# Kernel optimization log

Hardware: AMD Instinct MI355X
Metric: run time of the kernel (lower is better)

The kernel has to match this reference:

```python
import jax, jax.numpy as jnp
import numpy as np

N_EMBD = 2048
N_HEAD = 32
HEAD_SIZE = 64          # n_embd // n_head
MIX_DIM = 64            # RWKV-6 time-mix LoRA dim
DECAY_DIM = 128         # RWKV-6 decay LoRA dim
BATCH = 1024
STATE_ROWS = (2 + HEAD_SIZE) * 1  # single block, i = 0


def setup_inputs() -> dict:
    key = jax.random.key(0)
    ks = jax.random.split(key, 32)
    rn = lambda k, shp, s=0.02: jax.random.normal(k, shp, jnp.float32) * s
    d = {}
    d['x'] = jax.random.normal(ks[0], (BATCH, N_EMBD), jnp.float32)
    d['state'] = jax.random.normal(ks[1], (BATCH, STATE_ROWS, N_EMBD), jnp.float32) * 0.1
    d['ln1_w'] = jnp.ones((N_EMBD,), jnp.float32)
    d['ln1_b'] = jnp.zeros((N_EMBD,), jnp.float32)
    d['ln2_w'] = jnp.ones((N_EMBD,), jnp.float32)
    d['ln2_b'] = jnp.zeros((N_EMBD,), jnp.float32)
    d['maa_x'] = rn(ks[2], (N_EMBD,), 0.1)
    d['maa_w'] = rn(ks[3], (N_EMBD,), 0.1)
    d['maa_k'] = rn(ks[4], (N_EMBD,), 0.1)
    d['maa_v'] = rn(ks[5], (N_EMBD,), 0.1)
    d['maa_r'] = rn(ks[6], (N_EMBD,), 0.1)
    d['maa_g'] = rn(ks[7], (N_EMBD,), 0.1)
    d['maa_w1'] = rn(ks[8], (N_EMBD, 5 * MIX_DIM))
    d['maa_w2'] = rn(ks[9], (5, MIX_DIM, N_EMBD))
    d['decay'] = rn(ks[10], (N_EMBD,), 0.5) - 4.0  # typical negative log-decay
    d['decay_w1'] = rn(ks[11], (N_EMBD, DECAY_DIM))
    d['decay_w2'] = rn(ks[12], (DECAY_DIM, N_EMBD))
    d['faaaa'] = rn(ks[13], (N_HEAD, HEAD_SIZE, 1), 0.1)
    d['Wr'] = rn(ks[14], (N_EMBD, N_EMBD))
    d['Wk'] = rn(ks[15], (N_EMBD, N_EMBD))
    d['Wv'] = rn(ks[16], (N_EMBD, N_EMBD))
    d['Wo'] = rn(ks[17], (N_EMBD, N_EMBD))
    d['Wg'] = rn(ks[18], (N_EMBD, N_EMBD))
    d['gn_w'] = jnp.ones((N_EMBD,), jnp.float32)
    d['gn_b'] = jnp.zeros((N_EMBD,), jnp.float32)
    d['ffn_maa_k'] = rn(ks[19], (N_EMBD,), 0.1)
    d['ffn_maa_r'] = rn(ks[20], (N_EMBD,), 0.1)
    d['ffn_Wk'] = rn(ks[21], (N_EMBD, N_EMBD))
    d['ffn_Wr'] = rn(ks[22], (N_EMBD, N_EMBD))
    d['ffn_Wv'] = rn(ks[23], (N_EMBD, N_EMBD))
    d['i'] = 0
    return d


def _ln(x, w, b):
    mu = jnp.mean(x, -1, keepdims=True)
    var = jnp.var(x, -1, keepdims=True)
    return (x - mu) * jax.lax.rsqrt(var + 1e-5) * w + b


def reference(x, state, ln1_w, ln1_b, ln2_w, ln2_b,
              maa_x, maa_w, maa_k, maa_v, maa_r, maa_g, maa_w1, maa_w2,
              decay, decay_w1, decay_w2, faaaa,
              Wr, Wk, Wv, Wo, Wg, gn_w, gn_b,
              ffn_maa_k, ffn_maa_r, ffn_Wk, ffn_Wr, ffn_Wv, i):
    B = x.shape[0]
    H, S = N_HEAD, HEAD_SIZE
    # ---------------- time mixing ----------------
    xn = _ln(x, ln1_w, ln1_b)
    i1 = (2 + S) * i + 1
    sx = state[:, i1] - xn                                  # token shift delta
    xxx = xn + sx * maa_x
    xxx = jnp.tanh(xxx @ maa_w1).reshape(B, 5, 1, MIX_DIM)
    xxx = jnp.matmul(xxx, maa_w2).reshape(B, 5, N_EMBD)     # [B,5,E]
    mw, mk, mv, mr, mg = (xxx[:, j] for j in range(5))
    xw = xn + sx * (maa_w + mw)
    xk = xn + sx * (maa_k + mk)
    xv = xn + sx * (maa_v + mv)
    xr = xn + sx * (maa_r + mr)
    xg = xn + sx * (maa_g + mg)
    w = decay + jnp.tanh(xw @ decay_w1) @ decay_w2          # [B,E]
    w = jnp.exp(-jnp.exp(w.reshape(B, H, S, 1)))            # decay gate
    r = (xr @ Wr.T).reshape(B, H, 1, S)
    k = (xk @ Wk.T).reshape(B, H, S, 1)
    v = (xv @ Wv.T).reshape(B, H, 1, S)
    g = jax.nn.silu(xg @ Wg.T)
    s = state[:, (2 + S) * i + 2:(2 + S) * (i + 1), :].reshape(B, H, S, S)
    a = jnp.matmul(k, v)                                    # [B,H,S,S] outer product
    y = jnp.matmul(r, faaaa * a + s).reshape(B, N_EMBD)     # wkv readout
    # group norm (n_head groups over n_embd channels)
    yg = y.reshape(B, H, S)
    mu = jnp.mean(yg, -1, keepdims=True)
    var = jnp.var(yg, -1, keepdims=True)
    yg = ((yg - mu) * jax.lax.rsqrt(var + 1e-5)).reshape(B, N_EMBD) * gn_w + gn_b
    x1 = x + (yg * g) @ Wo.T
    # ---------------- channel mixing ----------------
    xn2 = _ln(x1, ln2_w, ln2_b)
    i0 = (2 + S) * i
    sx2 = state[:, i0] - xn2
    xk2 = xn2 + sx2 * ffn_maa_k
    xr2 = xn2 + sx2 * ffn_maa_r
    rr = jax.nn.sigmoid(xr2 @ ffn_Wr.T)
    kk = jnp.square(jax.nn.relu(xk2 @ ffn_Wk.T))
    return x1 + rr * (kk @ ffn_Wv.T)
```

## Files before the change

kernel.cpp:

```cpp
#include <hip/hip_runtime.h>
#include <cstdint>
#include <cstddef>

typedef unsigned short u16;
typedef __attribute__((ext_vector_type(8))) short bf16x8;
typedef __attribute__((ext_vector_type(4))) float f32x4;

#define DEV __device__ __forceinline__

DEV u16 f2bf(float f) {
  uint32_t b = __float_as_uint(f);
  b += 0x7fffu + ((b >> 16) & 1u);
  return (u16)(b >> 16);
}
DEV float bf2f(u16 u) { return __uint_as_float(((uint32_t)u) << 16); }

DEV void gl16(const u16* g, u16* l) {
  __builtin_amdgcn_global_load_lds(
      (const __attribute__((address_space(1))) void*)g,
      (__attribute__((address_space(3))) void*)l, 16, 0, 0);
}

struct CvtArgs { const float* s[8]; };

__global__ __launch_bounds__(256) void k_cvt8(CvtArgs a, u16* __restrict__ dst) {
  size_t idx = ((size_t)blockIdx.x * 256 + threadIdx.x) * 8;
  int w = (int)(idx >> 22);
  size_t off = idx & ((1u << 22) - 1);
  const float* s = a.s[w];
  float4 v0 = *(const float4*)(s + off);
  float4 v1 = *(const float4*)(s + off + 4);
  uint4 p; u16* pl = (u16*)&p;
  pl[0] = f2bf(v0.x); pl[1] = f2bf(v0.y); pl[2] = f2bf(v0.z); pl[3] = f2bf(v0.w);
  pl[4] = f2bf(v1.x); pl[5] = f2bf(v1.y); pl[6] = f2bf(v1.z); pl[7] = f2bf(v1.w);
  *(uint4*)(dst + ((size_t)w << 22) + off) = p;
}

__global__ __launch_bounds__(256) void k_cvtT(const float* __restrict__ w1,
                                              const float* __restrict__ w2,
                                              u16* __restrict__ w1t, u16* __restrict__ w2t) {
  int idx = blockIdx.x * 256 + threadIdx.x;
  if (idx < 655360) {
    int n = idx >> 11, k = idx & 2047;
    w1t[idx] = f2bf(w1[(size_t)k * 320 + n]);
  } else {
    int r = idx - 655360;
    int j = r >> 17, q = r & 131071;
    int n = q >> 6, k2 = q & 63;
    w2t[r] = f2bf(w2[((size_t)(j + 1) * 64 + k2) * 2048 + n]);
  }
}

__global__ __launch_bounds__(256) void k_tanhpack(const float* __restrict__ xf,
                                                  u16* __restrict__ xb) {
  int idx = blockIdx.x * 256 + threadIdx.x;
  xb[idx] = f2bf(tanhf(xf[idx]));
}

__global__ __launch_bounds__(256) void k_act(const float* __restrict__ rrf,
                                             const float* __restrict__ kkf,
                                             u16* __restrict__ rr, u16* __restrict__ kk) {
  int gid = blockIdx.x * 256 + threadIdx.x;
  int e0 = (gid & 262143) * 8;
  uint4 p; u16* pl = (u16*)&p;
  if (gid < 262144) {
    float4 v0 = *(const float4*)(rrf + e0);
    float4 v1 = *(const float4*)(rrf + e0 + 4);
    float vv[8] = {v0.x, v0.y, v0.z, v0.w, v1.x, v1.y, v1.z, v1.w};
#pragma unroll
    for (int j = 0; j < 8; ++j) pl[j] = f2bf(1.f / (1.f + __expf(-vv[j])));
    *(uint4*)(rr + e0) = p;
  } else {
    float4 v0 = *(const float4*)(kkf + e0);
    float4 v1 = *(const float4*)(kkf + e0 + 4);
    float vv[8] = {v0.x, v0.y, v0.z, v0.w, v1.x, v1.y, v1.z, v1.w};
#pragma unroll
    for (int j = 0; j < 8; ++j) { float r = vv[j] > 0.f ? vv[j] : 0.f; pl[j] = f2bf(r * r); }
    *(uint4*)(kk + e0) = p;
  }
}

__global__ __launch_bounds__(256) void k_ln_mix1(
    const float* __restrict__ x, const float* __restrict__ state,
    const int* __restrict__ ip,
    const float* __restrict__ lw, const float* __restrict__ lb,
    const float* __restrict__ mx,
    u16* __restrict__ xn_o, u16* __restrict__ sx_o, u16* __restrict__ a1_o,
    float* __restrict__ xxxf) {
  int b = blockIdx.x, t = threadIdx.x;
  float* zf = xxxf + (size_t)b * 320;
  zf[t] = 0.f;
  if (t < 64) zf[256 + t] = 0.f;
  const float* xr = x + (size_t)b * 2048;
  float4 v0 = *(const float4*)(xr + t * 8);
  float4 v1 = *(const float4*)(xr + t * 8 + 4);
  float xv[8] = {v0.x, v0.y, v0.z, v0.w, v1.x, v1.y, v1.z, v1.w};
  float s1 = 0.f, s2 = 0.f;
#pragma unroll
  for (int j = 0; j < 8; ++j) { s1 += xv[j]; s2 += xv[j] * xv[j]; }
#pragma unroll
  for (int off = 32; off; off >>= 1) { s1 += __shfl_xor(s1, off); s2 += __shfl_xor(s2, off); }
  __shared__ float ls1[4], ls2[4];
  int w = t >> 6;
  if ((t & 63) == 0) { ls1[w] = s1; ls2[w] = s2; }
  __syncthreads();
  s1 = ls1[0] + ls1[1] + ls1[2] + ls1[3];
  s2 = ls2[0] + ls2[1] + ls2[2] + ls2[3];
  float mu = s1 * (1.0f / 2048.0f);
  float var = s2 * (1.0f / 2048.0f) - mu * mu;
  float rs = rsqrtf(var + 1e-5f);
  const float* st = state + ((size_t)b * 66 + (size_t)66 * ip[0] + 1) * 2048;
  int e0 = t * 8;
  uint4 xnp, sxp, a1p;
  u16* xnl = (u16*)&xnp; u16* sxl = (u16*)&sxp; u16* a1l = (u16*)&a1p;
#pragma unroll
  for (int j = 0; j < 8; ++j) {
    int e = e0 + j;
    float xn = (xv[j] - mu) * rs * lw[e] + lb[e];
    float sxv = st[e] - xn;
    xnl[j] = f2bf(xn); sxl[j] = f2bf(sxv); a1l[j] = f2bf(xn + sxv * mx[e]);
  }
  size_t o = (size_t)b * 2048 + e0;
  *(uint4*)(xn_o + o) = xnp;
  *(uint4*)(sx_o + o) = sxp;
  *(uint4*)(a1_o + o) = a1p;
}

__global__ __launch_bounds__(256) void k_ln_mix2(
    const float* __restrict__ x1, const float* __restrict__ state,
    const int* __restrict__ ip,
    const float* __restrict__ lw, const float* __restrict__ lb,
    const float* __restrict__ mk, const float* __restrict__ mr,
    u16* __restrict__ xk_o, u16* __restrict__ xr_o, float* __restrict__ out) {
  int b = blockIdx.x, t = threadIdx.x;
  const float* xr = x1 + (size_t)b * 2048;
  float4 v0 = *(const float4*)(xr + t * 8);
  float4 v1 = *(const float4*)(xr + t * 8 + 4);
  float* op = out + (size_t)b * 2048 + t * 8;
  *(float4*)op = v0;
  *(float4*)(op + 4) = v1;
  float xv[8] = {v0.x, v0.y, v0.z, v0.w, v1.x, v1.y, v1.z, v1.w};
  float s1 = 0.f, s2 = 0.f;
#pragma unroll
  for (int j = 0; j < 8; ++j) { s1 += xv[j]; s2 += xv[j] * xv[j]; }
#pragma unroll
  for (int off = 32; off; off >>= 1) { s1 += __shfl_xor(s1, off); s2 += __shfl_xor(s2, off); }
  __shared__ float ls1[4], ls2[4];
  int w = t >> 6;
  if ((t & 63) == 0) { ls1[w] = s1; ls2[w] = s2; }
  __syncthreads();
  s1 = ls1[0] + ls1[1] + ls1[2] + ls1[3];
  s2 = ls2[0] + ls2[1] + ls2[2] + ls2[3];
  float mu = s1 * (1.0f / 2048.0f);
  float var = s2 * (1.0f / 2048.0f) - mu * mu;
  float rs = rsqrtf(var + 1e-5f);
  const float* st = state + ((size_t)b * 66 + (size_t)66 * ip[0] + 0) * 2048;
  int e0 = t * 8;
  uint4 xkp, xrp;
  u16* xkl = (u16*)&xkp; u16* xrl = (u16*)&xrp;
#pragma unroll
  for (int j = 0; j < 8; ++j) {
    int e = e0 + j;
    float xn = (xv[j] - mu) * rs * lw[e] + lb[e];
    float sxv = st[e] - xn;
    xkl[j] = f2bf(xn + sxv * mk[e]);
    xrl[j] = f2bf(xn + sxv * mr[e]);
  }
  size_t o = (size_t)b * 2048 + e0;
  *(uint4*)(xk_o + o) = xkp;
  *(uint4*)(xr_o + o) = xrp;
}

enum { EP_STORE = 0, EP_SILU, EP_MIX, EP_AT, EP_ATSC };

struct GemmDesc {
  const u16* A; const u16* B; void* C;
  const void* p1; const void* p2; const float* pvec;
  int lda, ldb, ldc, N, K, k0, ep;
};
struct GemmBatch { GemmDesc g[4]; int bpg; };

__global__ __launch_bounds__(256, 3) void k_gemm(GemmBatch bat) {
  int gi = blockIdx.x / bat.bpg;
  int bid = blockIdx.x % bat.bpg;
  GemmDesc g = bat.g[gi];
  int ntn = (g.N + 127) >> 7;
  int m0 = (bid / ntn) << 7;
  int n0 = (bid % ntn) << 7;
  __shared__ u16 As[2][128 * 32];
  __shared__ u16 Bs[2][128 * 32];
  int t = threadIdx.x, w = t >> 6, lane = t & 63;
  int wm = w >> 1, wn = w & 1;
  int lr = lane & 15, kb = (lane >> 4) * 8;
  const u16* Ab = g.A + (size_t)(m0 + w * 32 + (lane >> 2)) * g.lda + (lane & 3) * 8;
  const u16* Bb = g.B + (size_t)(n0 + w * 32 + (lane >> 2)) * g.ldb + (lane & 3) * 8;
  int a16 = 16 * g.lda, b16 = 16 * g.ldb;
  int aoff = (w * 32) * 32;
  f32x4 acc[4][4] = {};
  int nt = g.K >> 5;

  auto stage = [&](int buf, int kk) {
    u16* Ad = (u16*)As + buf * 4096 + aoff;
    u16* Bd = (u16*)Bs + buf * 4096 + aoff;
    gl16(Ab + kk, Ad);
    gl16(Ab + kk + a16, Ad + 512);
    gl16(Bb + kk, Bd);
    gl16(Bb + kk + b16, Bd + 512);
  };

  stage(0, g.k0);
  __syncthreads();
  int cur = 0;
  for (int ti = 0; ti < nt; ++ti) {
    if (ti + 1 < nt) stage(cur ^ 1, g.k0 + (ti + 1) * 32);
    const u16* Ac = (const u16*)As + cur * 4096;
    const u16* Bc = (const u16*)Bs + cur * 4096;
    bf16x8 af[4], bfr[4];
#pragma unroll
    for (int m = 0; m < 4; ++m)
      af[m] = *(const bf16x8*)(Ac + (wm * 64 + m * 16 + lr) * 32 + kb);
#pragma unroll
    for (int n = 0; n < 4; ++n)
      bfr[n] = *(const bf16x8*)(Bc + (wn * 64 + n * 16 + lr) * 32 + kb);
#pragma unroll
    for (int m = 0; m < 4; ++m)
#pragma unroll
      for (int n = 0; n < 4; ++n)
        acc[m][n] = __builtin_amdgcn_mfma_f32_16x16x32_bf16(af[m], bfr[n], acc[m][n], 0, 0, 0);
    __syncthreads();
    cur ^= 1;
  }

  int ep = g.ep;
#pragma unroll
  for (int m = 0; m < 4; ++m) {
    int grow0 = m0 + wm * 64 + m * 16 + (lane >> 4) * 4;
#pragma unroll
    for (int n = 0; n < 4; ++n) {
      int gc = n0 + wn * 64 + n * 16 + lr;
      if (gc >= g.N) continue;
#pragma unroll
      for (int q = 0; q < 4; ++q) {
        size_t ci = (size_t)(grow0 + q) * g.ldc + gc;
        float v = acc[m][n][q];
        switch (ep) {
          case EP_STORE: ((u16*)g.C)[ci] = f2bf(v); break;
          case EP_SILU:  ((u16*)g.C)[ci] = f2bf(v / (1.f + __expf(-v))); break;
          case EP_MIX: {
            float xn = bf2f(((const u16*)g.p1)[ci]);
            float sxv = bf2f(((const u16*)g.p2)[ci]);
            ((u16*)g.C)[ci] = f2bf(xn + sxv * (g.pvec[gc] + v));
          } break;
          case EP_AT:   atomicAdd((float*)g.C + ci, v); break;
          case EP_ATSC: atomicAdd((float*)g.C + ci, bf2f(((const u16*)g.p2)[ci]) * v); break;
        }
      }
    }
  }
}

__global__ __launch_bounds__(512, 2) void k_gemm2(GemmBatch bat) {
  extern __shared__ u16 lds[];
  int nwg = gridDim.x;
  int wg0 = blockIdx.x;
  int wg = (wg0 & 7) * (nwg >> 3) + (wg0 >> 3);
  int gi = wg / bat.bpg;
  int bid = wg % bat.bpg;
  GemmDesc g = bat.g[gi];
  int ntn = (g.N + 255) >> 8;
  int m0 = (bid / ntn) << 7;
  int n0 = (bid % ntn) << 8;
  int t = threadIdx.x, wv = t >> 6, lane = t & 63;
  int wm = wv >> 2, wn = wv & 3;
  int lr = lane & 15, hi = lane >> 4;

  const u16* asrc[2]; const u16* bsrc[4];
#pragma unroll
  for (int j = 0; j < 2; ++j) {
    int cid = t + 512 * j, r = cid >> 3, c = cid & 7;
    asrc[j] = g.A + (size_t)(m0 + r) * g.lda + ((c ^ (r & 7)) << 3);
  }
#pragma unroll
  for (int j = 0; j < 4; ++j) {
    int cid = t + 512 * j, r = cid >> 3, c = cid & 7;
    int rowB = n0 + r; if (rowB > g.N - 1) rowB = g.N - 1;
    bsrc[j] = g.B + (size_t)rowB * g.ldb + ((c ^ (r & 7)) << 3);
  }
  int au = wv * 512;

  auto stage = [&](int buf, int k) {
    u16* base = lds + buf * 24576;
#pragma unroll
    for (int j = 0; j < 2; ++j) gl16(asrc[j] + k, base + au + j * 4096);
#pragma unroll
    for (int j = 0; j < 4; ++j) gl16(bsrc[j] + k, base + 8192 + au + j * 4096);
  };

  int arow[4], brow[4];
#pragma unroll
  for (int m = 0; m < 4; ++m) arow[m] = wm * 64 + m * 16 + lr;
#pragma unroll
  for (int n = 0; n < 4; ++n) brow[n] = wn * 64 + n * 16 + lr;

  f32x4 acc[4][4] = {};
  int nt = g.K >> 6;
  stage(0, g.k0);
  if (nt > 1) stage(1, g.k0 + 64);

  for (int ti = 0; ti < nt; ++ti) {
    if (ti + 1 < nt) asm volatile("s_waitcnt vmcnt(6)" ::: "memory");
    else             asm volatile("s_waitcnt vmcnt(0)" ::: "memory");
    __builtin_amdgcn_sched_barrier(0);
    __builtin_amdgcn_s_barrier();
    __builtin_amdgcn_sched_barrier(0);
    const u16* buf = lds + (ti % 3) * 24576;
    bf16x8 af[4][2], bf[4][2];
#pragma unroll
    for (int m = 0; m < 4; ++m)
#pragma unroll
      for (int ks = 0; ks < 2; ++ks)
        af[m][ks] = *(const bf16x8*)(buf + arow[m] * 64 + ((((ks << 2) + hi) ^ (arow[m] & 7)) << 3));
#pragma unroll
    for (int n = 0; n < 4; ++n)
#pragma unroll
      for (int ks = 0; ks < 2; ++ks)
        bf[n][ks] = *(const bf16x8*)(buf + 8192 + brow[n] * 64 + ((((ks << 2) + hi) ^ (brow[n] & 7)) << 3));
    if (ti + 2 < nt) stage((ti + 2) % 3, g.k0 + (ti + 2) * 64);
    __builtin_amdgcn_s_setprio(1);
#pragma unroll
    for (int m = 0; m < 4; ++m)
#pragma unroll
      for (int n = 0; n < 4; ++n)
#pragma unroll
        for (int ks = 0; ks < 2; ++ks)
          acc[m][n] = __builtin_amdgcn_mfma_f32_16x16x32_bf16(af[m][ks], bf[n][ks], acc[m][n], 0, 0, 0);
    __builtin_amdgcn_s_setprio(0);
  }

  int ep = g.ep;
#pragma unroll
  for (int m = 0; m < 4; ++m) {
    int grow0 = m0 + wm * 64 + m * 16 + hi * 4;
#pragma unroll
    for (int n = 0; n < 4; ++n) {
      int gc = n0 + wn * 64 + n * 16 + lr;
      if (gc >= g.N) continue;
#pragma unroll
      for (int q = 0; q < 4; ++q) {
        size_t ci = (size_t)(grow0 + q) * g.ldc + gc;
        float v = acc[m][n][q];
        switch (ep) {
          case EP_STORE: ((u16*)g.C)[ci] = f2bf(v); break;
          case EP_SILU:  ((u16*)g.C)[ci] = f2bf(v / (1.f + __expf(-v))); break;
          case EP_AT:   atomicAdd((float*)g.C + ci, v); break;
          case EP_ATSC: atomicAdd((float*)g.C + ci, bf2f(((const u16*)g.p2)[ci]) * v); break;
          default: break;
        }
      }
    }
  }
}

__global__ __launch_bounds__(256) void k_wkv(
    const u16* __restrict__ rb, const u16* __restrict__ kbuf,
    const u16* __restrict__ vb, const u16* __restrict__ gb,
    const float* __restrict__ state, const int* __restrict__ ip,
    const float* __restrict__ fa, const float* __restrict__ gw,
    const float* __restrict__ gbias, u16* __restrict__ t_o,
    const float* __restrict__ x, float* __restrict__ x1,
    float* __restrict__ rrf, float* __restrict__ kkf) {
  int t = threadIdx.x, w = t >> 6, lane = t & 63;
  int gid = blockIdx.x * 256 + t;
  float4 z4 = make_float4(0.f, 0.f, 0.f, 0.f);
  if (gid < 524288) ((float4*)rrf)[gid] = z4;
  else if (gid < 1048576) ((float4*)kkf)[gid - 524288] = z4;
  int flat = blockIdx.x * 4 + w;
  int b = flat >> 5, h = flat & 31;
  int base = (b << 11) + (h << 6);
  x1[base + lane] = x[base + lane];
  float r  = bf2f(rb[base + lane]);
  float kv = bf2f(kbuf[base + lane]);
  float vv = bf2f(vb[base + lane]);
  float f  = fa[(h << 6) + lane];
  __shared__ float rs[4][64];
  rs[w][lane] = r;
  __syncthreads();
  float c = r * f * kv;
#pragma unroll
  for (int off = 32; off; off >>= 1) c += __shfl_xor(c, off);

  const float* sp = state + ((size_t)b * 66 + (size_t)66 * ip[0] + 2 + 2 * h) * 2048;
  int q = lane >> 4, jj = lane & 15;
  float yp0 = 0.f, yp1 = 0.f, yp2 = 0.f, yp3 = 0.f;
#pragma unroll
  for (int ib = 0; ib < 16; ++ib) {
    int i = ib * 4 + q;
    float4 sv = *(const float4*)(sp + ((i >> 5) * 2048) + ((i & 31) << 6) + jj * 4);
    float ri = rs[w][i];
    yp0 += ri * sv.x; yp1 += ri * sv.y; yp2 += ri * sv.z; yp3 += ri * sv.w;
  }
#pragma unroll
  for (int off = 16; off <= 32; off <<= 1) {
    yp0 += __shfl_xor(yp0, off); yp1 += __shfl_xor(yp1, off);
    yp2 += __shfl_xor(yp2, off); yp3 += __shfl_xor(yp3, off);
  }
  int src = lane >> 2, cc = lane & 3;
  float t0 = __shfl(yp0, src), t1 = __shfl(yp1, src);
  float t2 = __shfl(yp2, src), t3 = __shfl(yp3, src);
  float y = cc == 0 ? t0 : cc == 1 ? t1 : cc == 2 ? t2 : t3;
  y += c * vv;
  float s1 = y, s2 = y * y;
#pragma unroll
  for (int off = 32; off; off >>= 1) { s1 += __shfl_xor(s1, off); s2 += __shfl_xor(s2, off); }
  float mu = s1 * (1.f / 64.f);
  float var = s2 * (1.f / 64.f) - mu * mu;
  float yn = (y - mu) * rsqrtf(var + 1e-5f);
  float tg = (yn * gw[(h << 6) + lane] + gbias[(h << 6) + lane]) * bf2f(gb[base + lane]);
  t_o[base + lane] = f2bf(tg);
}

extern "C" void kernel_launch(void* const* d_in, const int* in_sizes, int n_in,
                              void* d_out, int out_size, void* d_ws, size_t ws_size,
                              hipStream_t stream) {
  const float* x      = (const float*)d_in[0];
  const float* state  = (const float*)d_in[1];
  const float* ln1_w  = (const float*)d_in[2];
  const float* ln1_b  = (const float*)d_in[3];
  const float* ln2_w  = (const float*)d_in[4];
  const float* ln2_b  = (const float*)d_in[5];
  const float* maa_x  = (const float*)d_in[6];
  const float* maa_k  = (const float*)d_in[8];
  const float* maa_v  = (const float*)d_in[9];
  const float* maa_r  = (const float*)d_in[10];
  const float* maa_g  = (const float*)d_in[11];
  const float* maa_w1 = (const float*)d_in[12];
  const float* maa_w2 = (const float*)d_in[13];
  const float* faaaa  = (const float*)d_in[17];
  const float* Wr     = (const float*)d_in[18];
  const float* Wk     = (const float*)d_in[19];
  const float* Wv     = (const float*)d_in[20];
  const float* Wo     = (const float*)d_in[21];
  const float* Wg     = (const float*)d_in[22];
  const float* gn_w   = (const float*)d_in[23];
  const float* gn_b   = (const float*)d_in[24];
  const float* fmk    = (const float*)d_in[25];
  const float* fmr    = (const float*)d_in[26];
  const float* fWk    = (const float*)d_in[27];
  const float* fWr    = (const float*)d_in[28];
  const float* fWv    = (const float*)d_in[29];
  const int*   ip     = (const int*)d_in[30];
  float* out = (float*)d_out;

  char* wsb = (char*)d_ws;
  const size_t MB = 1ull << 20;
  u16* wbf   = (u16*)(wsb + 0 * MB);
  u16* w1t   = (u16*)(wsb + 64 * MB);
  u16* w2t   = (u16*)(wsb + 66 * MB);
  u16* xn    = (u16*)(wsb + 68 * MB);
  u16* sx    = (u16*)(wsb + 72 * MB);
  u16* a1    = (u16*)(wsb + 76 * MB);
  float* xxxf = (float*)(wsb + 80 * MB);
  u16* xxx   = (u16*)(wsb + 82 * MB);
  u16* xk    = (u16*)(wsb + 83 * MB);
  u16* xv    = (u16*)(wsb + 87 * MB);
  u16* xr    = (u16*)(wsb + 91 * MB);
  u16* xg    = (u16*)(wsb + 95 * MB);
  u16* rb    = (u16*)(wsb + 99 * MB);
  u16* kb    = (u16*)(wsb + 103 * MB);
  u16* vbf   = (u16*)(wsb + 107 * MB);
  u16* gbf   = (u16*)(wsb + 111 * MB);
  u16* tb    = (u16*)(wsb + 115 * MB);
  float* x1  = (float*)(wsb + 119 * MB);
  u16* xk2   = (u16*)(wsb + 127 * MB);
  u16* xr2   = (u16*)(wsb + 131 * MB);
  u16* rr    = (u16*)(wsb + 135 * MB);
  u16* kkb   = (u16*)(wsb + 139 * MB);
  float* rrf = (float*)(wsb + 143 * MB);
  float* kkf = (float*)(wsb + 151 * MB);

  const size_t WSQ = 4194304;
  u16* bWr = wbf + 0 * WSQ; u16* bWk = wbf + 1 * WSQ; u16* bWv = wbf + 2 * WSQ;
  u16* bWg = wbf + 3 * WSQ; u16* bWo = wbf + 4 * WSQ; u16* bfWr = wbf + 5 * WSQ;
  u16* bfWk = wbf + 6 * WSQ; u16* bfWv = wbf + 7 * WSQ;

  auto mkd = [](const u16* A, const u16* B, void* C, const void* p1,
                const void* p2, const float* pvec, int lda, int ldb, int ldc,
                int N, int K, int k0, int epf) {
    GemmDesc d; d.A = A; d.B = B; d.C = C; d.p1 = p1; d.p2 = p2; d.pvec = pvec;
    d.lda = lda; d.ldb = ldb; d.ldc = ldc; d.N = N; d.K = K; d.k0 = k0; d.ep = epf;
    return d;
  };

  static const int LDS2 = 147456;
  hipFuncSetAttribute((const void*)k_gemm2,
                      hipFuncAttributeMaxDynamicSharedMemorySize, LDS2);

  {
    CvtArgs ca; ca.s[0] = Wr; ca.s[1] = Wk; ca.s[2] = Wv; ca.s[3] = Wg;
    ca.s[4] = Wo; ca.s[5] = fWr; ca.s[6] = fWk; ca.s[7] = fWv;
    k_cvt8<<<16384, 256, 0, stream>>>(ca, wbf);
    k_cvtT<<<4608, 256, 0, stream>>>(maa_w1, maa_w2, w1t, w2t);
  }

  k_ln_mix1<<<1024, 256, 0, stream>>>(x, state, ip, ln1_w, ln1_b, maa_x, xn, sx, a1, xxxf);

  {
    GemmBatch g{}; g.bpg = 8 * 3;
    for (int j = 0; j < 4; ++j)
      g.g[j] = mkd(a1, w1t, xxxf, nullptr, nullptr, nullptr, 2048, 2048, 320,
                   320, 512, j * 512, EP_AT);
    k_gemm<<<96, 256, 0, stream>>>(g);
  }
  k_tanhpack<<<1280, 256, 0, stream>>>(xxxf, xxx);

  {
    GemmBatch g{}; g.bpg = 8 * 16;
    const float* mv[4] = {maa_k, maa_v, maa_r, maa_g};
    u16* tv[4] = {xk, xv, xr, xg};
    for (int j = 1; j <= 4; ++j)
      g.g[j - 1] = mkd(xxx + j * 64, w2t + (size_t)(j - 1) * 131072, tv[j - 1],
                       xn, sx, mv[j - 1], 320, 64, 2048, 2048, 64, 0, EP_MIX);
    k_gemm<<<512, 256, 0, stream>>>(g);
  }

  {
    GemmBatch g{}; g.bpg = 8 * 8;
    g.g[0] = mkd(xr, bWr, rb,  nullptr, nullptr, nullptr, 2048, 2048, 2048, 2048, 2048, 0, EP_STORE);
    g.g[1] = mkd(xk, bWk, kb,  nullptr, nullptr, nullptr, 2048, 2048, 2048, 2048, 2048, 0, EP_STORE);
    g.g[2] = mkd(xv, bWv, vbf, nullptr, nullptr, nullptr, 2048, 2048, 2048, 2048, 2048, 0, EP_STORE);
    g.g[3] = mkd(xg, bWg, gbf, nullptr, nullptr, nullptr, 2048, 2048, 2048, 2048, 2048, 0, EP_SILU);
    k_gemm2<<<256, 512, LDS2, stream>>>(g);
  }

  k_wkv<<<8192, 256, 0, stream>>>(rb, kb, vbf, gbf, state, ip, faaaa, gn_w, gn_b, tb,
                                  x, x1, rrf, kkf);

  {
    GemmBatch g{}; g.bpg = 8 * 8;
    for (int j = 0; j < 4; ++j)
      g.g[j] = mkd(tb, bWo, x1, nullptr, nullptr, nullptr, 2048, 2048, 2048,
                   2048, 512, j * 512, EP_AT);
    k_gemm2<<<256, 512, LDS2, stream>>>(g);
  }

  k_ln_mix2<<<1024, 256, 0, stream>>>(x1, state, ip, ln2_w, ln2_b, fmk, fmr, xk2, xr2, out);

  {
    GemmBatch g{}; g.bpg = 8 * 8;
    g.g[0] = mkd(xr2, bfWr, rrf, nullptr, nullptr, nullptr, 2048, 2048, 2048, 2048, 1024, 0,    EP_AT);
    g.g[1] = mkd(xr2, bfWr, rrf, nullptr, nullptr, nullptr, 2048, 2048, 2048, 2048, 1024, 1024, EP_AT);
    g.g[2] = mkd(xk2, bfWk, kkf, nullptr, nullptr, nullptr, 2048, 2048, 2048, 2048, 1024, 0,    EP_AT);
    g.g[3] = mkd(xk2, bfWk, kkf, nullptr, nullptr, nullptr, 2048, 2048, 2048, 2048, 1024, 1024, EP_AT);
    k_gemm2<<<256, 512, LDS2, stream>>>(g);
  }
  k_act<<<2048, 256, 0, stream>>>(rrf, kkf, rr, kkb);

  {
    GemmBatch g{}; g.bpg = 8 * 8;
    for (int j = 0; j < 4; ++j)
      g.g[j] = mkd(kkb, bfWv, out, nullptr, rr, nullptr, 2048, 2048, 2048,
                   2048, 512, j * 512, EP_ATSC);
    k_gemm2<<<256, 512, LDS2, stream>>>(g);
  }
}
```

Before: 381.3 us.

## Replace atomic split-K accumulation with partial buffers reduced in consumer kernels

```diff
diff --git a/kernel.cpp b/kernel.cpp
--- a/kernel.cpp
+++ b/kernel.cpp
@@ -23,61 +23,98 @@
 
 struct CvtArgs { const float* s[8]; };
 
-__global__ __launch_bounds__(256) void k_cvt8(CvtArgs a, u16* __restrict__ dst) {
-  size_t idx = ((size_t)blockIdx.x * 256 + threadIdx.x) * 8;
-  int w = (int)(idx >> 22);
-  size_t off = idx & ((1u << 22) - 1);
-  const float* s = a.s[w];
-  float4 v0 = *(const float4*)(s + off);
-  float4 v1 = *(const float4*)(s + off + 4);
-  uint4 p; u16* pl = (u16*)&p;
-  pl[0] = f2bf(v0.x); pl[1] = f2bf(v0.y); pl[2] = f2bf(v0.z); pl[3] = f2bf(v0.w);
-  pl[4] = f2bf(v1.x); pl[5] = f2bf(v1.y); pl[6] = f2bf(v1.z); pl[7] = f2bf(v1.w);
-  *(uint4*)(dst + ((size_t)w << 22) + off) = p;
-}
-
-__global__ __launch_bounds__(256) void k_cvtT(const float* __restrict__ w1,
-                                              const float* __restrict__ w2,
-                                              u16* __restrict__ w1t, u16* __restrict__ w2t) {
-  int idx = blockIdx.x * 256 + threadIdx.x;
-  if (idx < 655360) {
-    int n = idx >> 11, k = idx & 2047;
-    w1t[idx] = f2bf(w1[(size_t)k * 320 + n]);
+__global__ __launch_bounds__(256) void k_cvt(CvtArgs a,
+                                             const float* __restrict__ w1,
+                                             const float* __restrict__ w2,
+                                             u16* __restrict__ dst,
+                                             u16* __restrict__ w1t,
+                                             u16* __restrict__ w2t) {
+  if (blockIdx.x < 16384) {
+    size_t idx = ((size_t)blockIdx.x * 256 + threadIdx.x) * 8;
+    int w = (int)(idx >> 22);
+    size_t off = idx & ((1u << 22) - 1);
+    const float* s = a.s[w];
+    float4 v0 = *(const float4*)(s + off);
+    float4 v1 = *(const float4*)(s + off + 4);
+    uint4 p; u16* pl = (u16*)&p;
+    pl[0] = f2bf(v0.x); pl[1] = f2bf(v0.y); pl[2] = f2bf(v0.z); pl[3] = f2bf(v0.w);
+    pl[4] = f2bf(v1.x); pl[5] = f2bf(v1.y); pl[6] = f2bf(v1.z); pl[7] = f2bf(v1.w);
+    *(uint4*)(dst + ((size_t)w << 22) + off) = p;
   } else {
-    int r = idx - 655360;
-    int j = r >> 17, q = r & 131071;
-    int n = q >> 6, k2 = q & 63;
-    w2t[r] = f2bf(w2[((size_t)(j + 1) * 64 + k2) * 2048 + n]);
-  }
-}
-
-__global__ __launch_bounds__(256) void k_tanhpack(const float* __restrict__ xf,
+    int idx = (blockIdx.x - 16384) * 256 + threadIdx.x;
+    if (idx < 655360) {
+      int n = idx >> 11, k = idx & 2047;
+      w1t[idx] = f2bf(w1[(size_t)k * 320 + n]);
+    } else {
+      int r = idx - 655360;
+      int j = r >> 17, q = r & 131071;
+      int n = q >> 6, k2 = q & 63;
+      w2t[r] = f2bf(w2[((size_t)(j + 1) * 64 + k2) * 2048 + n]);
+    }
+  }
+}
+
+__global__ __launch_bounds__(256) void k_tanhpack(const float* __restrict__ p2,
                                                   u16* __restrict__ xb) {
   int idx = blockIdx.x * 256 + threadIdx.x;
-  xb[idx] = f2bf(tanhf(xf[idx]));
-}
-
-__global__ __launch_bounds__(256) void k_act(const float* __restrict__ rrf,
-                                             const float* __restrict__ kkf,
+  float s = p2[idx] + p2[327680 + idx] + p2[2 * 327680 + idx] + p2[3 * 327680 + idx];
+  xb[idx] = f2bf(tanhf(s));
+}
+
+__global__ __launch_bounds__(256) void k_act(const float* __restrict__ p8,
                                              u16* __restrict__ rr, u16* __restrict__ kk) {
+  const size_t S = 2097152;
   int gid = blockIdx.x * 256 + threadIdx.x;
-  int e0 = (gid & 262143) * 8;
+  size_t e0 = (size_t)(gid & 262143) * 8;
+  int isk = gid >= 262144;
+  const float* base = p8 + (isk ? 4 * S : 0) + e0;
+  float acc[8];
+  {
+    float4 a0 = *(const float4*)base, a1 = *(const float4*)(base + 4);
+    acc[0] = a0.x; acc[1] = a0.y; acc[2] = a0.z; acc[3] = a0.w;
+    acc[4] = a1.x; acc[5] = a1.y; acc[6] = a1.z; acc[7] = a1.w;
+  }
+#pragma unroll
+  for (int s = 1; s < 4; ++s) {
+    const float* p = base + (size_t)s * S;
+    float4 a0 = *(const float4*)p, a1 = *(const float4*)(p + 4);
+    acc[0] += a0.x; acc[1] += a0.y; acc[2] += a0.z; acc[3] += a0.w;
+    acc[4] += a1.x; acc[5] += a1.y; acc[6] += a1.z; acc[7] += a1.w;
+  }
   uint4 p; u16* pl = (u16*)&p;
-  if (gid < 262144) {
-    float4 v0 = *(const float4*)(rrf + e0);
-    float4 v1 = *(const float4*)(rrf + e0 + 4);
-    float vv[8] = {v0.x, v0.y, v0.z, v0.w, v1.x, v1.y, v1.z, v1.w};
-#pragma unroll
-    for (int j = 0; j < 8; ++j) pl[j] = f2bf(1.f / (1.f + __expf(-vv[j])));
+  if (!isk) {
+#pragma unroll
+    for (int j = 0; j < 8; ++j) pl[j] = f2bf(1.f / (1.f + __expf(-acc[j])));
     *(uint4*)(rr + e0) = p;
   } else {
-    float4 v0 = *(const float4*)(kkf + e0);
-    float4 v1 = *(const float4*)(kkf + e0 + 4);
-    float vv[8] = {v0.x, v0.y, v0.z, v0.w, v1.x, v1.y, v1.z, v1.w};
-#pragma unroll
-    for (int j = 0; j < 8; ++j) { float r = vv[j] > 0.f ? vv[j] : 0.f; pl[j] = f2bf(r * r); }
+#pragma unroll
+    for (int j = 0; j < 8; ++j) { float r = acc[j] > 0.f ? acc[j] : 0.f; pl[j] = f2bf(r * r); }
     *(uint4*)(kk + e0) = p;
   }
+}
+
+__global__ __launch_bounds__(256) void k_fin(const float* __restrict__ x1,
+                                             const float* __restrict__ p9,
+                                             const u16* __restrict__ rr,
+                                             float* __restrict__ out) {
+  const size_t S = 2097152;
+  size_t e0 = ((size_t)blockIdx.x * 256 + threadIdx.x) * 8;
+  float acc[8] = {};
+#pragma unroll
+  for (int s = 0; s < 4; ++s) {
+    const float* p = p9 + (size_t)s * S + e0;
+    float4 a0 = *(const float4*)p, a1 = *(const float4*)(p + 4);
+    acc[0] += a0.x; acc[1] += a0.y; acc[2] += a0.z; acc[3] += a0.w;
+    acc[4] += a1.x; acc[5] += a1.y; acc[6] += a1.z; acc[7] += a1.w;
+  }
+  float4 x0 = *(const float4*)(x1 + e0), x4 = *(const float4*)(x1 + e0 + 4);
+  float xv[8] = {x0.x, x0.y, x0.z, x0.w, x4.x, x4.y, x4.z, x4.w};
+  uint4 rv = *(const uint4*)(rr + e0); u16* rl = (u16*)&rv;
+  float o[8];
+#pragma unroll
+  for (int j = 0; j < 8; ++j) o[j] = xv[j] + bf2f(rl[j]) * acc[j];
+  *(float4*)(out + e0) = make_float4(o[0], o[1], o[2], o[3]);
+  *(float4*)(out + e0 + 4) = make_float4(o[4], o[5], o[6], o[7]);
 }
 
 __global__ __launch_bounds__(256) void k_ln_mix1(
@@ -85,12 +122,8 @@
     const int* __restrict__ ip,
     const float* __restrict__ lw, const float* __restrict__ lb,
     const float* __restrict__ mx,
-    u16* __restrict__ xn_o, u16* __restrict__ sx_o, u16* __restrict__ a1_o,
-    float* __restrict__ xxxf) {
+    u16* __restrict__ xn_o, u16* __restrict__ sx_o, u16* __restrict__ a1_o) {
   int b = blockIdx.x, t = threadIdx.x;
-  float* zf = xxxf + (size_t)b * 320;
-  zf[t] = 0.f;
-  if (t < 64) zf[256 + t] = 0.f;
   const float* xr = x + (size_t)b * 2048;
   float4 v0 = *(const float4*)(xr + t * 8);
   float4 v1 = *(const float4*)(xr + t * 8 + 4);
@@ -127,24 +160,31 @@
 }
 
 __global__ __launch_bounds__(256) void k_ln_mix2(
-    const float* __restrict__ x1, const float* __restrict__ state,
-    const int* __restrict__ ip,
+    const float* __restrict__ x, const float* __restrict__ p6,
+    const float* __restrict__ state, const int* __restrict__ ip,
     const float* __restrict__ lw, const float* __restrict__ lb,
     const float* __restrict__ mk, const float* __restrict__ mr,
-    u16* __restrict__ xk_o, u16* __restrict__ xr_o, float* __restrict__ out) {
+    u16* __restrict__ xk_o, u16* __restrict__ xr_o, float* __restrict__ x1_o) {
+  const size_t S = 2097152;
   int b = blockIdx.x, t = threadIdx.x;
-  const float* xr = x1 + (size_t)b * 2048;
-  float4 v0 = *(const float4*)(xr + t * 8);
-  float4 v1 = *(const float4*)(xr + t * 8 + 4);
-  float* op = out + (size_t)b * 2048 + t * 8;
-  *(float4*)op = v0;
-  *(float4*)(op + 4) = v1;
+  size_t off = (size_t)b * 2048 + t * 8;
+  float4 v0 = *(const float4*)(x + off);
+  float4 v1 = *(const float4*)(x + off + 4);
   float xv[8] = {v0.x, v0.y, v0.z, v0.w, v1.x, v1.y, v1.z, v1.w};
+#pragma unroll
+  for (int s = 0; s < 4; ++s) {
+    const float* p = p6 + (size_t)s * S + off;
+    float4 a0 = *(const float4*)p, a1 = *(const float4*)(p + 4);
+    xv[0] += a0.x; xv[1] += a0.y; xv[2] += a0.z; xv[3] += a0.w;
+    xv[4] += a1.x; xv[5] += a1.y; xv[6] += a1.z; xv[7] += a1.w;
+  }
+  *(float4*)(x1_o + off) = make_float4(xv[0], xv[1], xv[2], xv[3]);
+  *(float4*)(x1_o + off + 4) = make_float4(xv[4], xv[5], xv[6], xv[7]);
   float s1 = 0.f, s2 = 0.f;
 #pragma unroll
   for (int j = 0; j < 8; ++j) { s1 += xv[j]; s2 += xv[j] * xv[j]; }
 #pragma unroll
-  for (int off = 32; off; off >>= 1) { s1 += __shfl_xor(s1, off); s2 += __shfl_xor(s2, off); }
+  for (int off2 = 32; off2; off2 >>= 1) { s1 += __shfl_xor(s1, off2); s2 += __shfl_xor(s2, off2); }
   __shared__ float ls1[4], ls2[4];
   int w = t >> 6;
   if ((t & 63) == 0) { ls1[w] = s1; ls2[w] = s2; }
@@ -166,19 +206,18 @@
     xkl[j] = f2bf(xn + sxv * mk[e]);
     xrl[j] = f2bf(xn + sxv * mr[e]);
   }
-  size_t o = (size_t)b * 2048 + e0;
-  *(uint4*)(xk_o + o) = xkp;
-  *(uint4*)(xr_o + o) = xrp;
-}
-
-enum { EP_STORE = 0, EP_SILU, EP_MIX, EP_AT, EP_ATSC };
+  *(uint4*)(xk_o + off) = xkp;
+  *(uint4*)(xr_o + off) = xrp;
+}
+
+enum { EP_STORE = 0, EP_SILU, EP_MIX, EP_STOREF };
 
 struct GemmDesc {
   const u16* A; const u16* B; void* C;
   const void* p1; const void* p2; const float* pvec;
   int lda, ldb, ldc, N, K, k0, ep;
 };
-struct GemmBatch { GemmDesc g[4]; int bpg; };
+struct GemmBatch { GemmDesc g[8]; int bpg; };
 
 __global__ __launch_bounds__(256, 3) void k_gemm(GemmBatch bat) {
   int gi = blockIdx.x / bat.bpg;
@@ -245,14 +284,13 @@
         float v = acc[m][n][q];
         switch (ep) {
           case EP_STORE: ((u16*)g.C)[ci] = f2bf(v); break;
-          case EP_SILU:  ((u16*)g.C)[ci] = f2bf(v / (1.f + __expf(-v))); break;
           case EP_MIX: {
             float xn = bf2f(((const u16*)g.p1)[ci]);
             float sxv = bf2f(((const u16*)g.p2)[ci]);
             ((u16*)g.C)[ci] = f2bf(xn + sxv * (g.pvec[gc] + v));
           } break;
-          case EP_AT:   atomicAdd((float*)g.C + ci, v); break;
-          case EP_ATSC: atomicAdd((float*)g.C + ci, bf2f(((const u16*)g.p2)[ci]) * v); break;
+          case EP_STOREF: ((float*)g.C)[ci] = v; break;
+          default: break;
         }
       }
     }
@@ -283,8 +321,7 @@
 #pragma unroll
   for (int j = 0; j < 4; ++j) {
     int cid = t + 512 * j, r = cid >> 3, c = cid & 7;
-    int rowB = n0 + r; if (rowB > g.N - 1) rowB = g.N - 1;
-    bsrc[j] = g.B + (size_t)rowB * g.ldb + ((c ^ (r & 7)) << 3);
+    bsrc[j] = g.B + (size_t)(n0 + r) * g.ldb + ((c ^ (r & 7)) << 3);
   }
   int au = wv * 512;
 
@@ -344,7 +381,6 @@
 #pragma unroll
     for (int n = 0; n < 4; ++n) {
       int gc = n0 + wn * 64 + n * 16 + lr;
-      if (gc >= g.N) continue;
 #pragma unroll
       for (int q = 0; q < 4; ++q) {
         size_t ci = (size_t)(grow0 + q) * g.ldc + gc;
@@ -352,8 +388,7 @@
         switch (ep) {
           case EP_STORE: ((u16*)g.C)[ci] = f2bf(v); break;
           case EP_SILU:  ((u16*)g.C)[ci] = f2bf(v / (1.f + __expf(-v))); break;
-          case EP_AT:   atomicAdd((float*)g.C + ci, v); break;
-          case EP_ATSC: atomicAdd((float*)g.C + ci, bf2f(((const u16*)g.p2)[ci]) * v); break;
+          case EP_STOREF: ((float*)g.C)[ci] = v; break;
           default: break;
         }
       }
@@ -361,26 +396,107 @@
   }
 }
 
+__global__ __launch_bounds__(512, 2) void k_gemm3(GemmBatch bat) {
+  extern __shared__ u16 lds[];
+  int nwg = gridDim.x;
+  int wg0 = blockIdx.x;
+  int wg = (wg0 & 7) * (nwg >> 3) + (wg0 >> 3);
+  GemmDesc g = bat.g[wg / bat.bpg];
+  int bid = wg % bat.bpg;
+  int ntn = g.N >> 8;
+  int m0 = (bid / ntn) << 8;
+  int n0 = (bid % ntn) << 8;
+  int t = threadIdx.x, wv = t >> 6, lane = t & 63;
+  int wm = wv >> 2, wn = wv & 3;
+  int lr = lane & 15, hi = lane >> 4;
+
+  const u16* asrc[4]; const u16* bsrc[4];
+#pragma unroll
+  for (int j = 0; j < 4; ++j) {
+    int cid = t + 512 * j, r = cid >> 3, c = cid & 7;
+    asrc[j] = g.A + (size_t)(m0 + r) * g.lda + ((c ^ (r & 7)) << 3);
+    bsrc[j] = g.B + (size_t)(n0 + r) * g.ldb + ((c ^ (r & 7)) << 3);
+  }
+  int au = wv * 512;
+
+  auto stage = [&](int buf, int k) {
+    u16* ab = lds + buf * 32768 + au;
+    u16* bb = lds + buf * 32768 + 16384 + au;
+#pragma unroll
+    for (int j = 0; j < 4; ++j) gl16(asrc[j] + k, ab + j * 4096);
+#pragma unroll
+    for (int j = 0; j < 4; ++j) gl16(bsrc[j] + k, bb + j * 4096);
+  };
+
+  int arow[8], brow[4];
+#pragma unroll
+  for (int m = 0; m < 8; ++m) arow[m] = wm * 128 + m * 16 + lr;
+#pragma unroll
+  for (int n = 0; n < 4; ++n) brow[n] = wn * 64 + n * 16 + lr;
+
+  f32x4 acc[8][4] = {};
+  int nt = g.K >> 6;
+  stage(0, g.k0);
+  if (nt > 1) stage(1, g.k0 + 64);
+
+  for (int ti = 0; ti < nt; ++ti) {
+    if (ti + 1 < nt) asm volatile("s_waitcnt vmcnt(8)" ::: "memory");
+    else             asm volatile("s_waitcnt vmcnt(0)" ::: "memory");
+    __builtin_amdgcn_sched_barrier(0);
+    __builtin_amdgcn_s_barrier();
+    __builtin_amdgcn_sched_barrier(0);
+    const u16* buf = lds + (ti & 1) * 32768;
+#pragma unroll
+    for (int ks = 0; ks < 2; ++ks) {
+      bf16x8 af[8], bf[4];
+#pragma unroll
+      for (int m = 0; m < 8; ++m)
+        af[m] = *(const bf16x8*)(buf + arow[m] * 64 + ((((ks << 2) + hi) ^ (arow[m] & 7)) << 3));
+#pragma unroll
+      for (int n = 0; n < 4; ++n)
+        bf[n] = *(const bf16x8*)(buf + 16384 + brow[n] * 64 + ((((ks << 2) + hi) ^ (brow[n] & 7)) << 3));
+      __builtin_amdgcn_s_setprio(1);
+#pragma unroll
+      for (int m = 0; m < 8; ++m)
+#pragma unroll
+        for (int n = 0; n < 4; ++n)
+          acc[m][n] = __builtin_amdgcn_mfma_f32_16x16x32_bf16(af[m], bf[n], acc[m][n], 0, 0, 0);
+      __builtin_amdgcn_s_setprio(0);
+    }
+    __builtin_amdgcn_sched_barrier(0);
+    __builtin_amdgcn_s_barrier();
+    __builtin_amdgcn_sched_barrier(0);
+    if (ti + 2 < nt) stage(ti & 1, g.k0 + (ti + 2) * 64);
+  }
+
+#pragma unroll
+  for (int m = 0; m < 8; ++m) {
+    int grow0 = m0 + wm * 128 + m * 16 + hi * 4;
+#pragma unroll
+    for (int n = 0; n < 4; ++n) {
+      int gc = n0 + wn * 64 + n * 16 + lr;
+#pragma unroll
+      for (int q = 0; q < 4; ++q)
+        ((float*)g.C)[(size_t)(grow0 + q) * g.ldc + gc] = acc[m][n][q];
+    }
+  }
+}
+
 __global__ __launch_bounds__(256) void k_wkv(
-    const u16* __restrict__ rb, const u16* __restrict__ kbuf,
-    const u16* __restrict__ vb, const u16* __restrict__ gb,
+    const float* __restrict__ p4,
     const float* __restrict__ state, const int* __restrict__ ip,
     const float* __restrict__ fa, const float* __restrict__ gw,
-    const float* __restrict__ gbias, u16* __restrict__ t_o,
-    const float* __restrict__ x, float* __restrict__ x1,
-    float* __restrict__ rrf, float* __restrict__ kkf) {
+    const float* __restrict__ gbias, u16* __restrict__ t_o) {
+  const size_t S = 2097152;
   int t = threadIdx.x, w = t >> 6, lane = t & 63;
-  int gid = blockIdx.x * 256 + t;
-  float4 z4 = make_float4(0.f, 0.f, 0.f, 0.f);
-  if (gid < 524288) ((float4*)rrf)[gid] = z4;
-  else if (gid < 1048576) ((float4*)kkf)[gid - 524288] = z4;
   int flat = blockIdx.x * 4 + w;
   int b = flat >> 5, h = flat & 31;
-  int base = (b << 11) + (h << 6);
-  x1[base + lane] = x[base + lane];
-  float r  = bf2f(rb[base + lane]);
-  float kv = bf2f(kbuf[base + lane]);
-  float vv = bf2f(vb[base + lane]);
+  size_t base = ((size_t)b << 11) + (h << 6) + lane;
+  float r  = p4[base] + p4[S + base];
+  float kv = p4[2 * S + base] + p4[3 * S + base];
+  float vv = p4[4 * S + base] + p4[5 * S + base];
+  float gs = p4[6 * S + base] + p4[7 * S + base];
+  float gg = gs / (1.f + __expf(-gs));
   float f  = fa[(h << 6) + lane];
   __shared__ float rs[4][64];
   rs[w][lane] = r;
@@ -415,8 +531,8 @@
   float mu = s1 * (1.f / 64.f);
   float var = s2 * (1.f / 64.f) - mu * mu;
   float yn = (y - mu) * rsqrtf(var + 1e-5f);
-  float tg = (yn * gw[(h << 6) + lane] + gbias[(h << 6) + lane]) * bf2f(gb[base + lane]);
-  t_o[base + lane] = f2bf(tg);
+  float tg = (yn * gw[(h << 6) + lane] + gbias[(h << 6) + lane]) * gg;
+  t_o[((size_t)b << 11) + (h << 6) + lane] = f2bf(tg);
 }
 
 extern "C" void kernel_launch(void* const* d_in, const int* in_sizes, int n_in,
@@ -459,59 +575,59 @@
   u16* xn    = (u16*)(wsb + 68 * MB);
   u16* sx    = (u16*)(wsb + 72 * MB);
   u16* a1    = (u16*)(wsb + 76 * MB);
-  float* xxxf = (float*)(wsb + 80 * MB);
-  u16* xxx   = (u16*)(wsb + 82 * MB);
-  u16* xk    = (u16*)(wsb + 83 * MB);
-  u16* xv    = (u16*)(wsb + 87 * MB);
-  u16* xr    = (u16*)(wsb + 91 * MB);
-  u16* xg    = (u16*)(wsb + 95 * MB);
-  u16* rb    = (u16*)(wsb + 99 * MB);
-  u16* kb    = (u16*)(wsb + 103 * MB);
-  u16* vbf   = (u16*)(wsb + 107 * MB);
-  u16* gbf   = (u16*)(wsb + 111 * MB);
-  u16* tb    = (u16*)(wsb + 115 * MB);
-  float* x1  = (float*)(wsb + 119 * MB);
-  u16* xk2   = (u16*)(wsb + 127 * MB);
-  u16* xr2   = (u16*)(wsb + 131 * MB);
-  u16* rr    = (u16*)(wsb + 135 * MB);
-  u16* kkb   = (u16*)(wsb + 139 * MB);
-  float* rrf = (float*)(wsb + 143 * MB);
-  float* kkf = (float*)(wsb + 151 * MB);
-
-  const size_t WSQ = 4194304;
+  float* p2  = (float*)(wsb + 80 * MB);
+  u16* xxx   = (u16*)(wsb + 86 * MB);
+  u16* xk    = (u16*)(wsb + 87 * MB);
+  u16* xv    = (u16*)(wsb + 91 * MB);
+  u16* xr    = (u16*)(wsb + 95 * MB);
+  u16* xg    = (u16*)(wsb + 99 * MB);
+  float* p4  = (float*)(wsb + 103 * MB);
+  u16* tb    = (u16*)(wsb + 167 * MB);
+  float* p6  = (float*)(wsb + 171 * MB);
+  float* x1  = (float*)(wsb + 203 * MB);
+  u16* xk2   = (u16*)(wsb + 211 * MB);
+  u16* xr2   = (u16*)(wsb + 215 * MB);
+  float* p8  = (float*)(wsb + 219 * MB);
+  u16* rr    = (u16*)(wsb + 283 * MB);
+  u16* kkb   = (u16*)(wsb + 287 * MB);
+  float* p9  = (float*)(wsb + 291 * MB);
+
+  const size_t WSQ = 4194304, S = 2097152;
   u16* bWr = wbf + 0 * WSQ; u16* bWk = wbf + 1 * WSQ; u16* bWv = wbf + 2 * WSQ;
   u16* bWg = wbf + 3 * WSQ; u16* bWo = wbf + 4 * WSQ; u16* bfWr = wbf + 5 * WSQ;
   u16* bfWk = wbf + 6 * WSQ; u16* bfWv = wbf + 7 * WSQ;
 
   auto mkd = [](const u16* A, const u16* B, void* C, const void* p1,
-                const void* p2, const float* pvec, int lda, int ldb, int ldc,
+                const void* p2_, const float* pvec, int lda, int ldb, int ldc,
                 int N, int K, int k0, int epf) {
-    GemmDesc d; d.A = A; d.B = B; d.C = C; d.p1 = p1; d.p2 = p2; d.pvec = pvec;
+    GemmDesc d; d.A = A; d.B = B; d.C = C; d.p1 = p1; d.p2 = p2_; d.pvec = pvec;
     d.lda = lda; d.ldb = ldb; d.ldc = ldc; d.N = N; d.K = K; d.k0 = k0; d.ep = epf;
     return d;
   };
 
   static const int LDS2 = 147456;
+  static const int LDS3 = 131072;
   hipFuncSetAttribute((const void*)k_gemm2,
                       hipFuncAttributeMaxDynamicSharedMemorySize, LDS2);
+  hipFuncSetAttribute((const void*)k_gemm3,
+                      hipFuncAttributeMaxDynamicSharedMemorySize, LDS3);
 
   {
     CvtArgs ca; ca.s[0] = Wr; ca.s[1] = Wk; ca.s[2] = Wv; ca.s[3] = Wg;
     ca.s[4] = Wo; ca.s[5] = fWr; ca.s[6] = fWk; ca.s[7] = fWv;
-    k_cvt8<<<16384, 256, 0, stream>>>(ca, wbf);
-    k_cvtT<<<4608, 256, 0, stream>>>(maa_w1, maa_w2, w1t, w2t);
-  }
-
-  k_ln_mix1<<<1024, 256, 0, stream>>>(x, state, ip, ln1_w, ln1_b, maa_x, xn, sx, a1, xxxf);
+    k_cvt<<<20992, 256, 0, stream>>>(ca, maa_w1, maa_w2, wbf, w1t, w2t);
+  }
+
+  k_ln_mix1<<<1024, 256, 0, stream>>>(x, state, ip, ln1_w, ln1_b, maa_x, xn, sx, a1);
 
   {
     GemmBatch g{}; g.bpg = 8 * 3;
     for (int j = 0; j < 4; ++j)
-      g.g[j] = mkd(a1, w1t, xxxf, nullptr, nullptr, nullptr, 2048, 2048, 320,
-                   320, 512, j * 512, EP_AT);
+      g.g[j] = mkd(a1, w1t, p2 + (size_t)j * 327680, nullptr, nullptr, nullptr,
+                   2048, 2048, 320, 320, 512, j * 512, EP_STOREF);
     k_gemm<<<96, 256, 0, stream>>>(g);
   }
-  k_tanhpack<<<1280, 256, 0, stream>>>(xxxf, xxx);
+  k_tanhpack<<<1280, 256, 0, stream>>>(p2, xxx);
 
   {
     GemmBatch g{}; g.bpg = 8 * 16;
@@ -524,42 +640,49 @@
   }
 
   {
+    GemmBatch g{}; g.bpg = 32;
+    const u16* av[4] = {xr, xk, xv, xg};
+    const u16* bv[4] = {bWr, bWk, bWv, bWg};
+    for (int q = 0; q < 4; ++q)
+      for (int s = 0; s < 2; ++s)
+        g.g[q * 2 + s] = mkd(av[q], bv[q], p4 + (size_t)(q * 2 + s) * S,
+                             nullptr, nullptr, nullptr, 2048, 2048, 2048,
+                             2048, 1024, s * 1024, EP_STOREF);
+    k_gemm3<<<256, 512, LDS3, stream>>>(g);
+  }
+
+  k_wkv<<<8192, 256, 0, stream>>>(p4, state, ip, faaaa, gn_w, gn_b, tb);
+
+  {
     GemmBatch g{}; g.bpg = 8 * 8;
-    g.g[0] = mkd(xr, bWr, rb,  nullptr, nullptr, nullptr, 2048, 2048, 2048, 2048, 2048, 0, EP_STORE);
-    g.g[1] = mkd(xk, bWk, kb,  nullptr, nullptr, nullptr, 2048, 2048, 2048, 2048, 2048, 0, EP_STORE);
-    g.g[2] = mkd(xv, bWv, vbf, nullptr, nullptr, nullptr, 2048, 2048, 2048, 2048, 2048, 0, EP_STORE);
-    g.g[3] = mkd(xg, bWg, gbf, nullptr, nullptr, nullptr, 2048, 2048, 2048, 2048, 2048, 0, EP_SILU);
+    for (int s = 0; s < 4; ++s)
+      g.g[s] = mkd(tb, bWo, p6 + (size_t)s * S, nullptr, nullptr, nullptr,
+                   2048, 2048, 2048, 2048, 512, s * 512, EP_STOREF);
     k_gemm2<<<256, 512, LDS2, stream>>>(g);
   }
 
-  k_wkv<<<8192, 256, 0, stream>>>(rb, kb, vbf, gbf, state, ip, faaaa, gn_w, gn_b, tb,
-                                  x, x1, rrf, kkf);
+  k_ln_mix2<<<1024, 256, 0, stream>>>(x, p6, state, ip, ln2_w, ln2_b, fmk, fmr,
+                                      xk2, xr2, x1);
+
+  {
+    GemmBatch g{}; g.bpg = 32;
+    for (int s = 0; s < 4; ++s) {
+      g.g[s]     = mkd(xr2, bfWr, p8 + (size_t)s * S, nullptr, nullptr, nullptr,
+                       2048, 2048, 2048, 2048, 512, s * 512, EP_STOREF);
+      g.g[4 + s] = mkd(xk2, bfWk, p8 + (size_t)(4 + s) * S, nullptr, nullptr, nullptr,
+                       2048, 2048, 2048, 2048, 512, s * 512, EP_STOREF);
+    }
+    k_gemm3<<<256, 512, LDS3, stream>>>(g);
+  }
+  k_act<<<2048, 256, 0, stream>>>(p8, rr, kkb);
 
   {
     GemmBatch g{}; g.bpg = 8 * 8;
-    for (int j = 0; j < 4; ++j)
-      g.g[j] = mkd(tb, bWo, x1, nullptr, nullptr, nullptr, 2048, 2048, 2048,
-                   2048, 512, j * 512, EP_AT);
+    for (int s = 0; s < 4; ++s)
+      g.g[s] = mkd(kkb, bfWv, p9 + (size_t)s * S, nullptr, nullptr, nullptr,
+                   2048, 2048, 2048, 2048, 512, s * 512, EP_STOREF);
     k_gemm2<<<256, 512, LDS2, stream>>>(g);
   }
 
-  k_ln_mix2<<<1024, 256, 0, stream>>>(x1, state, ip, ln2_w, ln2_b, fmk, fmr, xk2, xr2, out);
-
-  {
-    GemmBatch g{}; g.bpg = 8 * 8;
-    g.g[0] = mkd(xr2, bfWr, rrf, nullptr, nullptr, nullptr, 2048, 2048, 2048, 2048, 1024, 0,    EP_AT);
-    g.g[1] = mkd(xr2, bfWr, rrf, nullptr, nullptr, nullptr, 2048, 2048, 2048, 2048, 1024, 1024, EP_AT);
-    g.g[2] = mkd(xk2, bfWk, kkf, nullptr, nullptr, nullptr, 2048, 2048, 2048, 2048, 1024, 0,    EP_AT);
-    g.g[3] = mkd(xk2, bfWk, kkf, nullptr, nullptr, nullptr, 2048, 2048, 2048, 2048, 1024, 1024, EP_AT);
-    k_gemm2<<<256, 512, LDS2, stream>>>(g);
-  }
-  k_act<<<2048, 256, 0, stream>>>(rrf, kkf, rr, kkb);
-
-  {
-    GemmBatch g{}; g.bpg = 8 * 8;
-    for (int j = 0; j < 4; ++j)
-      g.g[j] = mkd(kkb, bfWv, out, nullptr, rr, nullptr, 2048, 2048, 2048,
-                   2048, 512, j * 512, EP_ATSC);
-    k_gemm2<<<256, 512, LDS2, stream>>>(g);
-  }
-}
+  k_fin<<<1024, 256, 0, stream>>>(x1, p9, rr, out);
+}
```

Result: faster. 355.1 us (-6.9%).
